# Kernel tuning notes

Measured on AMD Instinct MI355X. Metric: run time of the kernel, lower is better.

The kernel has to match this reference:

```python
import jax, jax.numpy as jnp
import numpy as np

DIM = 1024
HEAD = 16
HEAD_DIM = DIM // HEAD
B, S = 2, 2048
NEG = -1e9


def setup_inputs() -> dict:
    key = jax.random.key(0)
    k1, k2, k3 = jax.random.split(key, 3)
    x = jax.random.normal(k1, (B, S, DIM), dtype=jnp.float32)
    # torch nn.Linear(dim, 3*dim, bias=False): y = x @ W.T; store W.T directly
    W_qkv = jax.random.normal(k2, (DIM, 3 * DIM), dtype=jnp.float32) * (DIM ** -0.5)
    mask = jax.random.randint(k3, (B, S), 0, 2, dtype=jnp.int32)
    return {"x": x, "W_qkv": W_qkv, "mask": mask}


def reference(x, W_qkv, mask):
    b, s, _ = x.shape
    qkv = x @ W_qkv  # [b, s, 3*dim]
    q, k, v = jnp.split(qkv, 3, axis=-1)
    # 'b s (h d) -> b h s d'
    split_heads = lambda t: t.reshape(b, s, HEAD, HEAD_DIM).transpose(0, 2, 1, 3)
    q, k, v = split_heads(q), split_heads(k), split_heads(v)
    # NOTE: source applies NO 1/sqrt(d) scaling — kept faithful.
    scores = jnp.einsum('bhid,bhjd->bhij', q, k)  # [b, h, s, s]
    # mask 'b s -> b 1 1 s'; masked_fill where mask == 0
    scores = jnp.where(mask[:, None, None, :] == 0, jnp.float32(NEG), scores)
    attn = jax.nn.softmax(scores, axis=-1)
    out = jnp.einsum('bhij,bhjd->bhid', attn, v)  # [b, h, s, d]
    return out.transpose(0, 2, 1, 3).reshape(b, s, DIM)
```

## Files before the change

### kernel.cpp

```cpp
#include <hip/hip_runtime.h>

typedef _Float16 half8 __attribute__((ext_vector_type(8)));
typedef float f32x4 __attribute__((ext_vector_type(4)));

#define MFMA16(a, b, c) __builtin_amdgcn_mfma_f32_16x16x32_f16((a), (b), (c), 0, 0, 0)

static __device__ __forceinline__ unsigned short hfbits(float f) {
  return __builtin_bit_cast(unsigned short, (_Float16)f);
}

static __device__ __forceinline__ void gl16(const ushort* g, ushort* l) {
  __builtin_amdgcn_global_load_lds(
      (const __attribute__((address_space(1))) unsigned int*)g,
      (__attribute__((address_space(3))) unsigned int*)l, 16, 0, 0);
}

__global__ __launch_bounds__(256) void k_prep(const float* __restrict__ W,
                                              ushort* __restrict__ wt,
                                              const float* __restrict__ x,
                                              ushort* __restrict__ xh,
                                              const int* __restrict__ mask,
                                              float* __restrict__ biasc,
                                              int* __restrict__ cidx,
                                              int* __restrict__ nkvs) {
  __shared__ ushort tile[64][72];
  __shared__ int scnt[256];
  const int id = blockIdx.x;
  const int t = threadIdx.x;

  if (id >= 768) {
    const int pb = id - 768;
    const size_t p = ((size_t)pb * 256 + t) * 8;
    float4 a = *reinterpret_cast<const float4*>(x + p);
    float4 b = *reinterpret_cast<const float4*>(x + p + 4);
    union { ushort u[8]; uint4 v; } pk;
    pk.u[0] = hfbits(a.x); pk.u[1] = hfbits(a.y);
    pk.u[2] = hfbits(a.z); pk.u[3] = hfbits(a.w);
    pk.u[4] = hfbits(b.x); pk.u[5] = hfbits(b.y);
    pk.u[6] = hfbits(b.z); pk.u[7] = hfbits(b.w);
    *reinterpret_cast<uint4*>(xh + p) = pk.v;

    if (pb == 0) {
      for (int b = 0; b < 2; ++b) {
        const int* mb = mask + b * 2048;
        int mloc[8];
        int c = 0;
#pragma unroll
        for (int k = 0; k < 8; ++k) {
          mloc[k] = mb[t * 8 + k];
          c += (mloc[k] != 0);
        }
        scnt[t] = c;
        __syncthreads();
        for (int off = 1; off < 256; off <<= 1) {
          int v = scnt[t];
          int u = (t >= off) ? scnt[t - off] : 0;
          __syncthreads();
          scnt[t] = v + u;
          __syncthreads();
        }
        const int total = scnt[255];
        int p2 = scnt[t] - c;
#pragma unroll
        for (int k = 0; k < 8; ++k)
          if (mloc[k]) cidx[b * 2048 + (p2++)] = t * 8 + k;
        __syncthreads();
        for (int jc = t; jc < 2048; jc += 256) {
          if (jc >= total) cidx[b * 2048 + jc] = 0;
          biasc[b * 2048 + jc] = (jc < total) ? 0.f : -1e9f;
        }
        if (t == 0) {
          nkvs[b] = total;
          nkvs[2 + b] = ((total + 63) >> 6) << 6;
        }
        __syncthreads();
      }
    }
    return;
  }

  const int n0 = (id % 48) * 64, k0 = (id / 48) * 64;
#pragma unroll
  for (int i = 0; i < 4; ++i) {
    int p = t + i * 256;
    int r = p >> 4, c = (p & 15) << 2;
    float4 v = *reinterpret_cast<const float4*>(&W[(size_t)(k0 + r) * 3072 + n0 + c]);
    ushort4 u;
    u.x = hfbits(v.x); u.y = hfbits(v.y); u.z = hfbits(v.z); u.w = hfbits(v.w);
    *reinterpret_cast<ushort4*>(&tile[r][c]) = u;
  }
  __syncthreads();
#pragma unroll
  for (int i = 0; i < 4; ++i) {
    int p = t + i * 256;
    int rn = p >> 4, ck = (p & 15) << 2;
    ushort4 u;
    u.x = tile[ck + 0][rn]; u.y = tile[ck + 1][rn];
    u.z = tile[ck + 2][rn]; u.w = tile[ck + 3][rn];
    *reinterpret_cast<ushort4*>(&wt[(size_t)(n0 + rn) * 1024 + k0 + ck]) = u;
  }
}

__global__ __launch_bounds__(256) void k_gemm(const ushort* __restrict__ xh,
                                              const ushort* __restrict__ wt,
                                              ushort* __restrict__ qw,
                                              ushort* __restrict__ kw,
                                              ushort* __restrict__ vc,
                                              const int* __restrict__ cidx,
                                              const int* __restrict__ nkvs) {
  __shared__ __align__(16) ushort sA[128 * 64];
  __shared__ __align__(16) ushort sB[128 * 64];
  const int t = threadIdx.x;
  const int lane = t & 63, w = t >> 6;
  const int g = lane >> 4, lr = lane & 15;
  const int wr = w >> 1, wc = w & 1;

  const int id = blockIdx.x;
  int bn, batch = 0, mrow0 = 0;
  bool compact = false;
  if (id < 256) {
    bn = id & 7;
    mrow0 = (id >> 3) * 128;
  } else {
    const int kid = id - 256;
    bn = 8 + (kid & 15);
    const int bmc = kid >> 4;
    const int mt0 = (nkvs[0] + 127) >> 7;
    const int mt1 = (nkvs[1] + 127) >> 7;
    if (bmc < mt0) { batch = 0; mrow0 = bmc * 128; }
    else if (bmc < mt0 + mt1) { batch = 1; mrow0 = (bmc - mt0) * 128; }
    else return;
    compact = true;
  }

  int srow[4], soff[4];
  const ushort* asrc[4];
#pragma unroll
  for (int i = 0; i < 4; ++i) {
    const int c = 4 * w + i;
    const int r = c * 8 + (lane >> 3);
    const int sl = (lane & 7) ^ (((r & 3) << 1) ^ ((r >> 3) & 3));
    srow[i] = r;
    soff[i] = sl * 8;
    int arow;
    if (compact) arow = batch * 2048 + cidx[batch * 2048 + mrow0 + r];
    else arow = mrow0 + r;
    asrc[i] = xh + (size_t)arow * 1024 + soff[i];
  }

  int raswz[4], rbswz[4];
#pragma unroll
  for (int rs = 0; rs < 4; ++rs) {
    const int ra = wr * 64 + rs * 16 + lr;
    raswz[rs] = ((((ra & 3) << 1) ^ ((ra >> 3) & 3)) << 4);
    const int rb = wc * 64 + rs * 16 + lr;
    rbswz[rs] = ((((rb & 3) << 1) ^ ((rb >> 3) & 3)) << 4);
  }

  f32x4 acc[4][4] = {};

  for (int kt = 0; kt < 1024; kt += 64) {
#pragma unroll
    for (int i = 0; i < 4; ++i) {
      gl16(asrc[i] + kt, sA + (4 * w + i) * 512);
      gl16(wt + (size_t)(bn * 128 + srow[i]) * 1024 + kt + soff[i],
           sB + (4 * w + i) * 512);
    }
    __syncthreads();
#pragma unroll
    for (int ks = 0; ks < 64; ks += 32) {
      half8 af[4], bb[4];
#pragma unroll
      for (int rs = 0; rs < 4; ++rs) {
        const int ra = wr * 64 + rs * 16 + lr;
        af[rs] = *reinterpret_cast<const half8*>(
            (const char*)sA + ra * 128 + ((16 * g + 2 * ks) ^ raswz[rs]));
      }
#pragma unroll
      for (int cs = 0; cs < 4; ++cs) {
        const int rb = wc * 64 + cs * 16 + lr;
        bb[cs] = *reinterpret_cast<const half8*>(
            (const char*)sB + rb * 128 + ((16 * g + 2 * ks) ^ rbswz[cs]));
      }
#pragma unroll
      for (int rs = 0; rs < 4; ++rs)
#pragma unroll
        for (int cs = 0; cs < 4; ++cs)
          acc[rs][cs] = MFMA16(af[rs], bb[cs], acc[rs][cs]);
    }
    __syncthreads();
  }

  const int m0 = mrow0 + wr * 64;
  const int n0 = bn * 128 + wc * 64;
  const int which = n0 >> 10;
  const int h = (n0 >> 6) & 15;

  if (which == 2) {
    ushort* q = (w < 2) ? sA + w * 4096 : sB + (w - 2) * 4096;
#pragma unroll
    for (int rs = 0; rs < 4; ++rs)
#pragma unroll
      for (int r = 0; r < 4; ++r) {
        const int m = rs * 16 + g * 4 + r;
#pragma unroll
        for (int cs = 0; cs < 4; ++cs) {
          const int n = cs * 16 + lr;
          q[n * 64 + ((((m >> 3) ^ (n & 7)) << 3) | (m & 7))] =
              hfbits(acc[rs][cs][r]);
        }
      }
    ushort* vbase = vc + ((size_t)((batch << 4) + h) * 64) * 2048 + m0;
#pragma unroll
    for (int j = 0; j < 8; ++j) {
      const int dl = j * 8 + (lane >> 3);
      const int mc = lane & 7;
      uint4 vv = *reinterpret_cast<const uint4*>(
          q + dl * 64 + ((mc ^ (dl & 7)) << 3));
      *reinterpret_cast<uint4*>(vbase + (size_t)dl * 2048 + mc * 8) = vv;
    }
  } else if (which == 1) {
    ushort* dst = kw + ((size_t)((batch << 4) + h) * 2048) * 64;
#pragma unroll
    for (int rs = 0; rs < 4; ++rs) {
#pragma unroll
      for (int r = 0; r < 4; ++r) {
        const int s = m0 + rs * 16 + g * 4 + r;
        ushort* rowp = dst + (size_t)s * 64;
#pragma unroll
        for (int cs = 0; cs < 4; ++cs)
          rowp[cs * 16 + lr] = hfbits(acc[rs][cs][r]);
      }
    }
  } else {
#pragma unroll
    for (int rs = 0; rs < 4; ++rs) {
#pragma unroll
      for (int r = 0; r < 4; ++r) {
        int m = m0 + rs * 16 + g * 4 + r;
        int b = m >> 11, s = m & 2047;
        ushort* rowp = qw + ((size_t)((b << 4) + h) * 2048 + s) * 64;
#pragma unroll
        for (int cs = 0; cs < 4; ++cs)
          rowp[cs * 16 + lr] = hfbits(acc[rs][cs][r] * 1.44269504088896f);
      }
    }
  }
}

__global__ __launch_bounds__(512, 4) void k_attn(const ushort* __restrict__ qw,
                                                 const ushort* __restrict__ kw,
                                                 const ushort* __restrict__ vc,
                                                 const float* __restrict__ biasc,
                                                 const int* __restrict__ nkvs,
                                                 float* __restrict__ out) {
  __shared__ __align__(16) ushort sK[2][64][64];
  __shared__ __align__(16) ushort sV[2][64][64];

  const int t = threadIdx.x;
  const int lane = t & 63, w = t >> 6;
  const int g = lane >> 4, lr = lane & 15;

  const int id = blockIdx.x;
  const int j = id >> 3;
  const int bh = (id & 7) * 4 + (j >> 4);
  const int qblk = j & 15;
  const int b = bh >> 4, h = bh & 15;

  const int ntk = nkvs[2 + b];

  const int qrow = qblk * 128 + w * 16 + lr;
  const ushort* qp = qw + ((size_t)bh * 2048 + qrow) * 64;
  const half8 qb0 = *reinterpret_cast<const half8*>(qp + g * 8);
  const half8 qb1 = *reinterpret_cast<const half8*>(qp + 32 + g * 8);

  const ushort* kbh = kw + (size_t)bh * 2048 * 64;
  const ushort* vbh = vc + (size_t)bh * 64 * 2048;
  const float* biasb = biasc + b * 2048;

  const int krbase = (lr >> 2) * 8 + (lr & 3);
  const int kswz = (((lr & 3) << 1) ^ (lr >> 2)) << 4;

  const int sr0 = w * 8 + (lane >> 3);
  const int scb = (lane & 7) << 4;
  const int swz0 = scb ^ ((((sr0 & 3) << 1) ^ ((sr0 >> 3) & 3)) << 4);

  auto stage = [&](int bufi, int jtn) {
    gl16(kbh + (size_t)(jtn + sr0) * 64 + (swz0 >> 1), &sK[bufi][0][0] + w * 512);
    gl16(vbh + (size_t)sr0 * 2048 + jtn + (swz0 >> 1), &sV[bufi][0][0] + w * 512);
  };

  const half8 vones = {(_Float16)1.f, (_Float16)1.f, (_Float16)1.f, (_Float16)1.f,
                       (_Float16)1.f, (_Float16)1.f, (_Float16)1.f, (_Float16)1.f};

  float m_run = -__builtin_inff();
  f32x4 o[4] = {};
  f32x4 oden = {};

  stage(0, 0);
  __syncthreads();
  int buf = 0;

  for (int jt = 0; jt < ntk; jt += 64) {
    if (jt + 64 < ntk) stage(buf ^ 1, jt + 64);

    f32x4 bias4[4];
#pragma unroll
    for (int jn = 0; jn < 4; ++jn) {
      const int koff = (jn & 1) * 4 + (jn >> 1) * 32;
      bias4[jn] = *reinterpret_cast<const f32x4*>(biasb + jt + koff + g * 8);
    }

    half8 vf0[4], vf1[4];
#pragma unroll
    for (int dn = 0; dn < 4; ++dn) {
      const int vr = dn * 16 + lr;
      const int vswz = ((((lr & 3) << 1) ^ ((2 * dn + (lr >> 3)) & 3)) << 4);
      const char* vrow = (const char*)&sV[buf][vr][0];
      vf0[dn] = *reinterpret_cast<const half8*>(vrow + ((16 * g) ^ vswz));
      vf1[dn] = *reinterpret_cast<const half8*>(vrow + ((64 + 16 * g) ^ vswz));
    }

    float st[4][4];
#pragma unroll
    for (int jn = 0; jn < 4; ++jn) {
      const int koff = (jn & 1) * 4 + (jn >> 1) * 32;
      const int kr = koff + krbase;
      const char* krow = (const char*)&sK[buf][kr][0];
      half8 ka0 = *reinterpret_cast<const half8*>(krow + ((16 * g) ^ kswz));
      half8 ka1 = *reinterpret_cast<const half8*>(krow + ((64 + 16 * g) ^ kswz));
      f32x4 s4 = bias4[jn];
      s4 = MFMA16(ka0, qb0, s4);
      s4 = MFMA16(ka1, qb1, s4);
#pragma unroll
      for (int r = 0; r < 4; ++r) st[jn][r] = s4[r];
    }

    float ma = fmaxf(fmaxf(st[0][0], st[0][1]), st[0][2]);
    ma = fmaxf(fmaxf(ma, st[0][3]), st[1][0]);
    ma = fmaxf(fmaxf(ma, st[1][1]), st[1][2]);
    ma = fmaxf(ma, st[1][3]);
    float mb2 = fmaxf(fmaxf(st[2][0], st[2][1]), st[2][2]);
    mb2 = fmaxf(fmaxf(mb2, st[2][3]), st[3][0]);
    mb2 = fmaxf(fmaxf(mb2, st[3][1]), st[3][2]);
    mb2 = fmaxf(mb2, st[3][3]);
    float tmax = fmaxf(ma, mb2);
    tmax = fmaxf(tmax, __shfl_xor(tmax, 16));
    tmax = fmaxf(tmax, __shfl_xor(tmax, 32));

    if (!__all(tmax <= m_run + 8.f)) {
      const float mnew = fmaxf(m_run, tmax);
      const float sc = __builtin_amdgcn_exp2f(m_run - mnew);
      const float s0 = __shfl(sc, g * 4 + 0);
      const float s1 = __shfl(sc, g * 4 + 1);
      const float s2 = __shfl(sc, g * 4 + 2);
      const float s3 = __shfl(sc, g * 4 + 3);
#pragma unroll
      for (int dn = 0; dn < 4; ++dn) {
        o[dn][0] *= s0; o[dn][1] *= s1; o[dn][2] *= s2; o[dn][3] *= s3;
      }
      oden[0] *= s0; oden[1] *= s1; oden[2] *= s2; oden[3] *= s3;
      m_run = mnew;
    }

    unsigned int pd[8];
#pragma unroll
    for (int jn = 0; jn < 4; ++jn) {
      float p0 = __builtin_amdgcn_exp2f(st[jn][0] - m_run);
      float p1 = __builtin_amdgcn_exp2f(st[jn][1] - m_run);
      float p2 = __builtin_amdgcn_exp2f(st[jn][2] - m_run);
      float p3 = __builtin_amdgcn_exp2f(st[jn][3] - m_run);
      pd[jn * 2 + 0] = __builtin_bit_cast(unsigned int, __builtin_amdgcn_cvt_pkrtz(p0, p1));
      pd[jn * 2 + 1] = __builtin_bit_cast(unsigned int, __builtin_amdgcn_cvt_pkrtz(p2, p3));
    }

    union { unsigned int u[4]; half8 h; } pa0u, pa1u;
    pa0u.u[0] = pd[0]; pa0u.u[1] = pd[1]; pa0u.u[2] = pd[2]; pa0u.u[3] = pd[3];
    pa1u.u[0] = pd[4]; pa1u.u[1] = pd[5]; pa1u.u[2] = pd[6]; pa1u.u[3] = pd[7];

    __builtin_amdgcn_s_setprio(1);
#pragma unroll
    for (int dn = 0; dn < 4; ++dn) {
      o[dn] = MFMA16(pa0u.h, vf0[dn], o[dn]);
      o[dn] = MFMA16(pa1u.h, vf1[dn], o[dn]);
    }
    oden = MFMA16(pa0u.h, vones, oden);
    oden = MFMA16(pa1u.h, vones, oden);
    __builtin_amdgcn_s_setprio(0);

    __syncthreads();
    buf ^= 1;
  }

  const float i0 = 1.f / oden[0];
  const float i1 = 1.f / oden[1];
  const float i2 = 1.f / oden[2];
  const float i3 = 1.f / oden[3];
  const int s0r = qblk * 128 + w * 16 + g * 4;
  float* ob = out + ((size_t)b * 2048 + s0r) * 1024 + h * 64;
#pragma unroll
  for (int dn = 0; dn < 4; ++dn) {
    ob[0 * 1024 + dn * 16 + lr] = o[dn][0] * i0;
    ob[1 * 1024 + dn * 16 + lr] = o[dn][1] * i1;
    ob[2 * 1024 + dn * 16 + lr] = o[dn][2] * i2;
    ob[3 * 1024 + dn * 16 + lr] = o[dn][3] * i3;
  }
}

extern "C" void kernel_launch(void* const* d_in, const int* in_sizes, int n_in,
                              void* d_out, int out_size, void* d_ws, size_t ws_size,
                              hipStream_t stream) {
  const float* x = (const float*)d_in[0];
  const float* W = (const float*)d_in[1];
  const int* mask = (const int*)d_in[2];
  float* out = (float*)d_out;
  char* ws = (char*)d_ws;

  ushort* wt = (ushort*)(ws);
  ushort* qw = (ushort*)(ws + 6291456);
  ushort* kw = (ushort*)(ws + 6291456 + 8388608);
  ushort* xh = (ushort*)(ws + 6291456 + 2 * (size_t)8388608);
  ushort* vc = (ushort*)(ws + 6291456 + 3 * (size_t)8388608);
  char* tail = ws + 6291456 + 4 * (size_t)8388608;
  float* biasc = (float*)(tail);
  int* cidx = (int*)(tail + 16384);
  int* nkvs = (int*)(tail + 32768);

  k_prep<<<dim3(2816), 256, 0, stream>>>(W, wt, x, xh, mask, biasc, cidx, nkvs);
  k_gemm<<<dim3(768), 256, 0, stream>>>(xh, wt, qw, kw, vc, cidx, nkvs);
  k_attn<<<dim3(512), 512, 0, stream>>>(qw, kw, vc, biasc, nkvs, out);
}
```

Baseline: 85.52 us.

## Double-buffer QKV GEMM LDS tiles and remap blocks for XCD locality

The QKV projection GEMM now uses two LDS buffers per operand, prefetching the next K-tile via global_load_lds while computing the current one, with explicit vmcnt waits and raw s_barrier. Block indices are also remapped so blocks sharing an XCD work on neighboring row/column tiles, improving L2 reuse of A and B tiles. This doubles LDS use to 64KB per block, which may reduce occupancy. The epilogue staging pointer is adjusted to the new buffer layout.

```diff
diff --git a/kernel.cpp b/kernel.cpp
--- a/kernel.cpp
+++ b/kernel.cpp
@@ -108,8 +108,8 @@
                                               ushort* __restrict__ vc,
                                               const int* __restrict__ cidx,
                                               const int* __restrict__ nkvs) {
-  __shared__ __align__(16) ushort sA[128 * 64];
-  __shared__ __align__(16) ushort sB[128 * 64];
+  __shared__ __align__(16) ushort sA[2][128 * 64];
+  __shared__ __align__(16) ushort sB[2][128 * 64];
   const int t = threadIdx.x;
   const int lane = t & 63, w = t >> 6;
   const int g = lane >> 4, lr = lane & 15;
@@ -119,12 +119,14 @@
   int bn, batch = 0, mrow0 = 0;
   bool compact = false;
   if (id < 256) {
-    bn = id & 7;
-    mrow0 = (id >> 3) * 128;
+    const int xcd = id & 7, wi = id >> 3;
+    bn = (xcd & 1) * 4 + (wi & 3);
+    mrow0 = ((xcd >> 1) * 8 + (wi >> 2)) * 128;
   } else {
     const int kid = id - 256;
-    bn = 8 + (kid & 15);
-    const int bmc = kid >> 4;
+    const int xcd = kid & 7, wi = kid >> 3;
+    bn = 8 + (xcd & 1) * 8 + (wi & 7);
+    const int bmc = (wi >> 3) * 4 + (xcd >> 1);
     const int mt0 = (nkvs[0] + 127) >> 7;
     const int mt1 = (nkvs[1] + 127) >> 7;
     if (bmc < mt0) { batch = 0; mrow0 = bmc * 128; }
@@ -157,16 +159,30 @@
     rbswz[rs] = ((((rb & 3) << 1) ^ ((rb >> 3) & 3)) << 4);
   }
 
+  auto stage = [&](int bi, int kt) {
+#pragma unroll
+    for (int i = 0; i < 4; ++i) {
+      gl16(asrc[i] + kt, sA[bi] + (4 * w + i) * 512);
+      gl16(wt + (size_t)(bn * 128 + srow[i]) * 1024 + kt + soff[i],
+           sB[bi] + (4 * w + i) * 512);
+    }
+  };
+
   f32x4 acc[4][4] = {};
 
-  for (int kt = 0; kt < 1024; kt += 64) {
-#pragma unroll
-    for (int i = 0; i < 4; ++i) {
-      gl16(asrc[i] + kt, sA + (4 * w + i) * 512);
-      gl16(wt + (size_t)(bn * 128 + srow[i]) * 1024 + kt + soff[i],
-           sB + (4 * w + i) * 512);
-    }
-    __syncthreads();
+  stage(0, 0);
+  for (int it = 0; it < 16; ++it) {
+    if (it < 15) {
+      stage((it + 1) & 1, (it + 1) * 64);
+      asm volatile("s_waitcnt vmcnt(8)" ::: "memory");
+    } else {
+      asm volatile("s_waitcnt vmcnt(0)" ::: "memory");
+    }
+    __builtin_amdgcn_sched_barrier(0);
+    __builtin_amdgcn_s_barrier();
+    __builtin_amdgcn_sched_barrier(0);
+
+    const int cb = it & 1;
 #pragma unroll
     for (int ks = 0; ks < 64; ks += 32) {
       half8 af[4], bb[4];
@@ -174,13 +190,13 @@
       for (int rs = 0; rs < 4; ++rs) {
         const int ra = wr * 64 + rs * 16 + lr;
         af[rs] = *reinterpret_cast<const half8*>(
-            (const char*)sA + ra * 128 + ((16 * g + 2 * ks) ^ raswz[rs]));
+            (const char*)sA[cb] + ra * 128 + ((16 * g + 2 * ks) ^ raswz[rs]));
       }
 #pragma unroll
       for (int cs = 0; cs < 4; ++cs) {
         const int rb = wc * 64 + cs * 16 + lr;
         bb[cs] = *reinterpret_cast<const half8*>(
-            (const char*)sB + rb * 128 + ((16 * g + 2 * ks) ^ rbswz[cs]));
+            (const char*)sB[cb] + rb * 128 + ((16 * g + 2 * ks) ^ rbswz[cs]));
       }
 #pragma unroll
       for (int rs = 0; rs < 4; ++rs)
@@ -188,7 +204,9 @@
         for (int cs = 0; cs < 4; ++cs)
           acc[rs][cs] = MFMA16(af[rs], bb[cs], acc[rs][cs]);
     }
-    __syncthreads();
+    __builtin_amdgcn_sched_barrier(0);
+    __builtin_amdgcn_s_barrier();
+    __builtin_amdgcn_sched_barrier(0);
   }
 
   const int m0 = mrow0 + wr * 64;
@@ -197,7 +215,7 @@
   const int h = (n0 >> 6) & 15;
 
   if (which == 2) {
-    ushort* q = (w < 2) ? sA + w * 4096 : sB + (w - 2) * 4096;
+    ushort* q = sA[0] + w * 4096;
 #pragma unroll
     for (int rs = 0; rs < 4; ++rs)
 #pragma unroll
```

New measurement: 80.85 us. 5.5% less time.
